# Kernel optimization log

Hardware: AMD Instinct MI355X
Metric: run time of the kernel (lower is better)

## Reference

```python
import jax, jax.numpy as jnp
import numpy as np

B, T, DIN = 256, 2048, 3
H = 128
DOUT = 26


def _slstm_layer(x_seq, W, R, b):
    """sLSTM layer with exponential gating + log-domain stabilizer.
    x_seq: (B, T, Din); W: (4H, Din); R: (4H, H); b: (4H,). Returns (B, T, H)."""
    # input-driven gate preactivations for all timesteps at once
    gx = jnp.einsum('btd,gd->btg', x_seq, W) + b  # (B, T, 4H)
    gx = jnp.swapaxes(gx, 0, 1)                    # (T, B, 4H)
    Bsz = x_seq.shape[0]
    Hd = R.shape[1]
    z0 = jnp.zeros((Bsz, Hd), x_seq.dtype)

    def step(carry, gx_t):
        h, c, n, m = carry
        g = gx_t + h @ R.T                         # (B, 4H)
        it, ft, zt, ot = jnp.split(g, 4, axis=-1)
        m_new = jnp.maximum(ft + m, it)            # stabilizer state
        i = jnp.exp(it - m_new)                    # stabilized exp input gate
        f = jnp.exp(ft + m - m_new)                # stabilized exp forget gate
        z = jnp.tanh(zt)
        o = jax.nn.sigmoid(ot)
        c_new = f * c + i * z
        n_new = f * n + i                          # normalizer state
        h_new = o * (c_new / n_new)
        return (h_new, c_new, n_new, m_new), h_new

    (_, _, _, _), hs = jax.lax.scan(step, (z0, z0, z0, z0), gx)
    return jnp.swapaxes(hs, 0, 1)                  # (B, T, H)


def setup_inputs() -> dict:
    key = jax.random.key(0)
    ks = jax.random.split(key, 12)
    s = 0.1
    x = jax.random.normal(ks[0], (B, T, DIN), dtype=jnp.float32)
    W0 = jax.random.normal(ks[1], (4 * H, DIN), dtype=jnp.float32) * s
    R0 = jax.random.normal(ks[2], (4 * H, H), dtype=jnp.float32) * s
    b0 = jax.random.normal(ks[3], (4 * H,), dtype=jnp.float32) * s
    W1 = jax.random.normal(ks[4], (4 * H, H), dtype=jnp.float32) * s
    R1 = jax.random.normal(ks[5], (4 * H, H), dtype=jnp.float32) * s
    b1 = jax.random.normal(ks[6], (4 * H,), dtype=jnp.float32) * s
    Wmu = jax.random.normal(ks[7], (DOUT, H), dtype=jnp.float32) * s
    bmu = jax.random.normal(ks[8], (DOUT,), dtype=jnp.float32) * s
    Wsig = jax.random.normal(ks[9], (DOUT, H), dtype=jnp.float32) * s
    bsig = jax.random.normal(ks[10], (DOUT,), dtype=jnp.float32) * s
    return {"x": x, "W0": W0, "R0": R0, "b0": b0, "W1": W1, "R1": R1,
            "b1": b1, "Wmu": Wmu, "bmu": bmu, "Wsig": Wsig, "bsig": bsig}


def reference(x, W0, R0, b0, W1, R1, b1, Wmu, bmu, Wsig, bsig):
    h1 = _slstm_layer(x, W0, R0, b0)     # (B, T, H)
    h2 = _slstm_layer(h1, W1, R1, b1)    # (B, T, H)
    last = h2[:, -1, :]                  # (B, H); dropout is identity in eval
    mu = last @ Wmu.T + bmu
    sigma = jax.nn.softplus(last @ Wsig.T + bsig) + 1e-6
    return mu, sigma
```

## Files before the change

### kernel.cpp

```cpp
#include <hip/hip_runtime.h>
#include <cmath>

#define TT    2048
#define HH    128
#define G4    512
#define NDIN  3
#define NDOUT 26
#define NTHR  512

typedef _Float16 h2t __attribute__((ext_vector_type(2)));
typedef _Float16 h8t __attribute__((ext_vector_type(8)));

__device__ __forceinline__ float fdot2(h2t a, h2t b, float c) {
    return __builtin_amdgcn_fdot2(a, b, c, false);
}

union H8u { h8t v; h2t h[4]; };

__device__ __forceinline__ float fast_rcp(float x) { return __builtin_amdgcn_rcpf(x); }

__global__
__attribute__((amdgpu_flat_work_group_size(NTHR, NTHR), amdgpu_waves_per_eu(2, 2)))
void slstm2_kernel(
    const float* __restrict__ x,
    const float* __restrict__ W0, const float* __restrict__ R0, const float* __restrict__ b0,
    const float* __restrict__ W1, const float* __restrict__ R1, const float* __restrict__ b1,
    const float* __restrict__ Wmu, const float* __restrict__ bmu,
    const float* __restrict__ Wsig, const float* __restrict__ bsig,
    float* __restrict__ out, int B)
{
    const int b = blockIdx.x;
    const int j = threadIdx.x;

    __shared__ float xs[TT * NDIN];
    __shared__ __align__(16) _Float16 h1h[HH];
    __shared__ __align__(16) _Float16 h2h[HH];
    __shared__ float g1[G4];
    __shared__ float g2[G4];
    __shared__ float h2f[HH];

    const float* xb = x + (size_t)b * (TT * NDIN);
    #pragma unroll
    for (int r = 0; r < (TT * NDIN) / NTHR; ++r)
        xs[r * NTHR + j] = xb[r * NTHR + j];

    h2t wr0[64], ww1[64], wr1[64];
    {
        const float4* r0p = (const float4*)(R0 + (size_t)j * HH);
        const float4* w1p = (const float4*)(W1 + (size_t)j * HH);
        const float4* r1p = (const float4*)(R1 + (size_t)j * HH);
        #pragma unroll
        for (int k = 0; k < 32; ++k) {
            float4 a = r0p[k];
            h2t t0 = {(_Float16)a.x, (_Float16)a.y};
            h2t t1 = {(_Float16)a.z, (_Float16)a.w};
            wr0[2*k] = t0; wr0[2*k+1] = t1;
            float4 c = w1p[k];
            h2t t2 = {(_Float16)c.x, (_Float16)c.y};
            h2t t3 = {(_Float16)c.z, (_Float16)c.w};
            ww1[2*k] = t2; ww1[2*k+1] = t3;
            float4 d = r1p[k];
            h2t t4 = {(_Float16)d.x, (_Float16)d.y};
            h2t t5 = {(_Float16)d.z, (_Float16)d.w};
            wr1[2*k] = t4; wr1[2*k+1] = t5;
        }
    }
    const float w0a = W0[j*NDIN+0], w0b = W0[j*NDIN+1], w0c = W0[j*NDIN+2];
    const float b0j = b0[j], b1j = b1[j];

    if (j < HH) { h1h[j] = (_Float16)0.f; h2h[j] = (_Float16)0.f; }
    float c_s = 0.f, n_s = 0.f, m_s = 0.f, hlast = 0.f;

    __syncthreads();

    const h8t* h1p = (const h8t*)h1h;
    const h8t* h2p = (const h8t*)h2h;

    for (int t = 0; t <= TT; ++t) {
        const int tc = (t < TT) ? t : (TT - 1);
        const float xv0 = xs[tc*3+0], xv1 = xs[tc*3+1], xv2 = xs[tc*3+2];

        float a0=0.f,a1=0.f,a2=0.f,a3=0.f;
        float d0=0.f,d1=0.f,d2=0.f,d3=0.f;
        float e0=0.f,e1=0.f,e2=0.f,e3=0.f;
        #pragma unroll
        for (int kk = 0; kk < 16; ++kk) {
            H8u u1, u2;
            u1.v = h1p[kk];
            u2.v = h2p[kk];
            a0 = fdot2(wr0[4*kk+0], u1.h[0], a0);
            a1 = fdot2(wr0[4*kk+1], u1.h[1], a1);
            a2 = fdot2(wr0[4*kk+2], u1.h[2], a2);
            a3 = fdot2(wr0[4*kk+3], u1.h[3], a3);
            d0 = fdot2(ww1[4*kk+0], u1.h[0], d0);
            d1 = fdot2(ww1[4*kk+1], u1.h[1], d1);
            d2 = fdot2(ww1[4*kk+2], u1.h[2], d2);
            d3 = fdot2(ww1[4*kk+3], u1.h[3], d3);
            e0 = fdot2(wr1[4*kk+0], u2.h[0], e0);
            e1 = fdot2(wr1[4*kk+1], u2.h[1], e1);
            e2 = fdot2(wr1[4*kk+2], u2.h[2], e2);
            e3 = fdot2(wr1[4*kk+3], u2.h[3], e3);
        }
        g1[j] = b0j + w0a*xv0 + w0b*xv1 + w0c*xv2 + ((a0+a1)+(a2+a3));
        g2[j] = b1j + ((d0+d1)+(d2+d3)) + ((e0+e1)+(e2+e3));
        __syncthreads();

        if (t < TT && j < HH) {
            const float it = g1[j], ft = g1[HH+j], zt = g1[2*HH+j], ot = g1[3*HH+j];
            const float mn = fmaxf(ft + m_s, it);
            const float iv = __expf(it - mn);
            const float fv = __expf(ft + m_s - mn);
            const float tq = __expf(-2.f * fabsf(zt));
            float zv = (1.f - tq) * fast_rcp(1.f + tq);
            zv = (zt < 0.f) ? -zv : zv;
            const float ov = fast_rcp(1.f + __expf(-ot));
            c_s = fv * c_s + iv * zv;
            n_s = fv * n_s + iv;
            m_s = mn;
            const float hv = ov * (c_s * fast_rcp(n_s));
            h1h[j] = (_Float16)hv;
        } else if (t > 0 && j >= HH && j < 2*HH) {
            const int e = j - HH;
            const float it = g2[e], ft = g2[HH+e], zt = g2[2*HH+e], ot = g2[3*HH+e];
            const float mn = fmaxf(ft + m_s, it);
            const float iv = __expf(it - mn);
            const float fv = __expf(ft + m_s - mn);
            const float tq = __expf(-2.f * fabsf(zt));
            float zv = (1.f - tq) * fast_rcp(1.f + tq);
            zv = (zt < 0.f) ? -zv : zv;
            const float ov = fast_rcp(1.f + __expf(-ot));
            c_s = fv * c_s + iv * zv;
            n_s = fv * n_s + iv;
            m_s = mn;
            const float hv = ov * (c_s * fast_rcp(n_s));
            hlast = hv;
            h2h[e] = (_Float16)hv;
        }
        __syncthreads();
    }

    if (j >= HH && j < 2*HH) h2f[j - HH] = hlast;
    __syncthreads();

    if (j < 2 * NDOUT) {
        const int d = (j < NDOUT) ? j : (j - NDOUT);
        const float* Wr = ((j < NDOUT) ? Wmu : Wsig) + (size_t)d * HH;
        float acc = (j < NDOUT) ? bmu[d] : bsig[d];
        #pragma unroll 8
        for (int k = 0; k < HH; ++k) acc += h2f[k] * Wr[k];
        if (j < NDOUT) {
            out[(size_t)b * NDOUT + d] = acc;
        } else {
            const float sp = fmaxf(acc, 0.f) + log1pf(__expf(-fabsf(acc)));
            out[(size_t)B * NDOUT + (size_t)b * NDOUT + d] = sp + 1e-6f;
        }
    }
}

extern "C" void kernel_launch(void* const* d_in, const int* in_sizes, int n_in,
                              void* d_out, int out_size, void* d_ws, size_t ws_size,
                              hipStream_t stream) {
    const float* x    = (const float*)d_in[0];
    const float* W0   = (const float*)d_in[1];
    const float* R0   = (const float*)d_in[2];
    const float* b0   = (const float*)d_in[3];
    const float* W1   = (const float*)d_in[4];
    const float* R1   = (const float*)d_in[5];
    const float* b1   = (const float*)d_in[6];
    const float* Wmu  = (const float*)d_in[7];
    const float* bmu  = (const float*)d_in[8];
    const float* Wsig = (const float*)d_in[9];
    const float* bsig = (const float*)d_in[10];
    float* out = (float*)d_out;

    const int B = in_sizes[0] / (TT * NDIN);

    slstm2_kernel<<<B, NTHR, 0, stream>>>(x, W0, R0, b0, W1, R1, b1,
                                          Wmu, bmu, Wsig, bsig, out, B);
}
```

Measured before the change: 2.430 ms.

## Replace per-thread fdot2 recurrent matvecs with MFMA 16x16x32 f16 tiles

Moves the per-step recurrent matvecs (R0·h1, W1·h1, R1·h2) from per-thread fdot2 loops onto MFMA 16x16x32 instructions, with weight fragments held in registers. Gates are regrouped so the four gates of each hidden unit land together in shared memory. Since the B operand is a single broadcast h vector, most of each MFMA's output columns are redundant and only lane m==0 stores results. The input projection and biases are precomputed into shared tables and applied in the gate stage. The concatenated h buffer serves both layers.

```diff
diff --git a/kernel.cpp b/kernel.cpp
--- a/kernel.cpp
+++ b/kernel.cpp
@@ -3,25 +3,27 @@
 
 #define TT    2048
 #define HH    128
-#define G4    512
 #define NDIN  3
 #define NDOUT 26
 #define NTHR  512
 
-typedef _Float16 h2t __attribute__((ext_vector_type(2)));
-typedef _Float16 h8t __attribute__((ext_vector_type(8)));
-
-__device__ __forceinline__ float fdot2(h2t a, h2t b, float c) {
-    return __builtin_amdgcn_fdot2(a, b, c, false);
+typedef _Float16 f16x8 __attribute__((ext_vector_type(8)));
+typedef float    f32x4 __attribute__((ext_vector_type(4)));
+
+__device__ __forceinline__ float fast_rcp(float x){ return __builtin_amdgcn_rcpf(x); }
+
+__device__ __forceinline__ f16x8 cvt8(const float* __restrict__ p){
+    float4 a = *(const float4*)p;
+    float4 b = *(const float4*)(p+4);
+    f16x8 r;
+    r[0]=(_Float16)a.x; r[1]=(_Float16)a.y; r[2]=(_Float16)a.z; r[3]=(_Float16)a.w;
+    r[4]=(_Float16)b.x; r[5]=(_Float16)b.y; r[6]=(_Float16)b.z; r[7]=(_Float16)b.w;
+    return r;
 }
-
-union H8u { h8t v; h2t h[4]; };
-
-__device__ __forceinline__ float fast_rcp(float x) { return __builtin_amdgcn_rcpf(x); }
 
 __global__
 __attribute__((amdgpu_flat_work_group_size(NTHR, NTHR), amdgpu_waves_per_eu(2, 2)))
-void slstm2_kernel(
+void slstm2_mfma(
     const float* __restrict__ x,
     const float* __restrict__ W0, const float* __restrict__ R0, const float* __restrict__ b0,
     const float* __restrict__ W1, const float* __restrict__ R1, const float* __restrict__ b1,
@@ -29,84 +31,121 @@
     const float* __restrict__ Wsig, const float* __restrict__ bsig,
     float* __restrict__ out, int B)
 {
-    const int b = blockIdx.x;
-    const int j = threadIdx.x;
+    const int b    = blockIdx.x;
+    const int tid  = threadIdx.x;
+    const int wave = tid >> 6;
+    const int lane = tid & 63;
+    const int m    = lane & 15;
+    const int g    = lane >> 4;
 
     __shared__ float xs[TT * NDIN];
-    __shared__ __align__(16) _Float16 h1h[HH];
-    __shared__ __align__(16) _Float16 h2h[HH];
-    __shared__ float g1[G4];
-    __shared__ float g2[G4];
+    __shared__ __align__(16) _Float16 hcat[2 * HH];
+    __shared__ __align__(16) float g1q[HH * 4];
+    __shared__ __align__(16) float g2q[HH * 4];
+    __shared__ __align__(16) float w0g[4][HH * 4];
+    __shared__ __align__(16) float b1qs[HH * 4];
     __shared__ float h2f[HH];
 
     const float* xb = x + (size_t)b * (TT * NDIN);
     #pragma unroll
     for (int r = 0; r < (TT * NDIN) / NTHR; ++r)
-        xs[r * NTHR + j] = xb[r * NTHR + j];
-
-    h2t wr0[64], ww1[64], wr1[64];
-    {
-        const float4* r0p = (const float4*)(R0 + (size_t)j * HH);
-        const float4* w1p = (const float4*)(W1 + (size_t)j * HH);
-        const float4* r1p = (const float4*)(R1 + (size_t)j * HH);
-        #pragma unroll
-        for (int k = 0; k < 32; ++k) {
-            float4 a = r0p[k];
-            h2t t0 = {(_Float16)a.x, (_Float16)a.y};
-            h2t t1 = {(_Float16)a.z, (_Float16)a.w};
-            wr0[2*k] = t0; wr0[2*k+1] = t1;
-            float4 c = w1p[k];
-            h2t t2 = {(_Float16)c.x, (_Float16)c.y};
-            h2t t3 = {(_Float16)c.z, (_Float16)c.w};
-            ww1[2*k] = t2; ww1[2*k+1] = t3;
-            float4 d = r1p[k];
-            h2t t4 = {(_Float16)d.x, (_Float16)d.y};
-            h2t t5 = {(_Float16)d.z, (_Float16)d.w};
-            wr1[2*k] = t4; wr1[2*k+1] = t5;
-        }
-    }
-    const float w0a = W0[j*NDIN+0], w0b = W0[j*NDIN+1], w0c = W0[j*NDIN+2];
-    const float b0j = b0[j], b1j = b1[j];
-
-    if (j < HH) { h1h[j] = (_Float16)0.f; h2h[j] = (_Float16)0.f; }
+        xs[r * NTHR + tid] = xb[r * NTHR + tid];
+
+    if (tid < HH) {
+        #pragma unroll
+        for (int q = 0; q < 4; ++q) {
+            w0g[q][tid*4+0] = W0[(q*HH + tid)*NDIN + 0];
+            w0g[q][tid*4+1] = W0[(q*HH + tid)*NDIN + 1];
+            w0g[q][tid*4+2] = W0[(q*HH + tid)*NDIN + 2];
+            w0g[q][tid*4+3] = b0[q*HH + tid];
+            b1qs[tid*4+q]   = b1[q*HH + tid];
+        }
+        hcat[tid] = (_Float16)0.f;
+        hcat[HH + tid] = (_Float16)0.f;
+    }
+
+    f16x8 a1[4][4];
+    f16x8 a2[4][8];
+    #pragma unroll
+    for (int tl = 0; tl < 4; ++tl) {
+        const int e = (wave*4 + tl)*4 + (m >> 2);
+        const int q = m & 3;
+        const size_t row = (size_t)(q*HH + e);
+        #pragma unroll
+        for (int kt = 0; kt < 4; ++kt)
+            a1[tl][kt] = cvt8(R0 + row*HH + kt*32 + g*8);
+        #pragma unroll
+        for (int kt = 0; kt < 4; ++kt)
+            a2[tl][kt] = cvt8(W1 + row*HH + kt*32 + g*8);
+        #pragma unroll
+        for (int kt = 0; kt < 4; ++kt)
+            a2[tl][4+kt] = cvt8(R1 + row*HH + kt*32 + g*8);
+    }
+
     float c_s = 0.f, n_s = 0.f, m_s = 0.f, hlast = 0.f;
-
     __syncthreads();
 
-    const h8t* h1p = (const h8t*)h1h;
-    const h8t* h2p = (const h8t*)h2h;
-
     for (int t = 0; t <= TT; ++t) {
-        const int tc = (t < TT) ? t : (TT - 1);
-        const float xv0 = xs[tc*3+0], xv1 = xs[tc*3+1], xv2 = xs[tc*3+2];
-
-        float a0=0.f,a1=0.f,a2=0.f,a3=0.f;
-        float d0=0.f,d1=0.f,d2=0.f,d3=0.f;
-        float e0=0.f,e1=0.f,e2=0.f,e3=0.f;
-        #pragma unroll
-        for (int kk = 0; kk < 16; ++kk) {
-            H8u u1, u2;
-            u1.v = h1p[kk];
-            u2.v = h2p[kk];
-            a0 = fdot2(wr0[4*kk+0], u1.h[0], a0);
-            a1 = fdot2(wr0[4*kk+1], u1.h[1], a1);
-            a2 = fdot2(wr0[4*kk+2], u1.h[2], a2);
-            a3 = fdot2(wr0[4*kk+3], u1.h[3], a3);
-            d0 = fdot2(ww1[4*kk+0], u1.h[0], d0);
-            d1 = fdot2(ww1[4*kk+1], u1.h[1], d1);
-            d2 = fdot2(ww1[4*kk+2], u1.h[2], d2);
-            d3 = fdot2(ww1[4*kk+3], u1.h[3], d3);
-            e0 = fdot2(wr1[4*kk+0], u2.h[0], e0);
-            e1 = fdot2(wr1[4*kk+1], u2.h[1], e1);
-            e2 = fdot2(wr1[4*kk+2], u2.h[2], e2);
-            e3 = fdot2(wr1[4*kk+3], u2.h[3], e3);
-        }
-        g1[j] = b0j + w0a*xv0 + w0b*xv1 + w0c*xv2 + ((a0+a1)+(a2+a3));
-        g2[j] = b1j + ((d0+d1)+(d2+d3)) + ((e0+e1)+(e2+e3));
+        f16x8 bf[4];
+        #pragma unroll
+        for (int kt = 0; kt < 4; ++kt)
+            bf[kt] = *(const f16x8*)(hcat + kt*32 + g*8);
+
+        f32x4 cL1[4];
+        #pragma unroll
+        for (int tl = 0; tl < 4; ++tl) cL1[tl] = f32x4{0.f,0.f,0.f,0.f};
+        #pragma unroll
+        for (int kt = 0; kt < 4; ++kt) {
+            #pragma unroll
+            for (int tl = 0; tl < 4; ++tl)
+                cL1[tl] = __builtin_amdgcn_mfma_f32_16x16x32_f16(a1[tl][kt], bf[kt], cL1[tl], 0, 0, 0);
+        }
+        if (m == 0) {
+            #pragma unroll
+            for (int tl = 0; tl < 4; ++tl) {
+                const int e = (wave*4 + tl)*4 + g;
+                *(f32x4*)(g1q + e*4) = cL1[tl];
+            }
+        }
+
+        f32x4 cL2[4];
+        #pragma unroll
+        for (int tl = 0; tl < 4; ++tl) cL2[tl] = f32x4{0.f,0.f,0.f,0.f};
+        #pragma unroll
+        for (int kt = 0; kt < 4; ++kt) {
+            #pragma unroll
+            for (int tl = 0; tl < 4; ++tl)
+                cL2[tl] = __builtin_amdgcn_mfma_f32_16x16x32_f16(a2[tl][kt], bf[kt], cL2[tl], 0, 0, 0);
+        }
+        #pragma unroll
+        for (int kt = 0; kt < 4; ++kt)
+            bf[kt] = *(const f16x8*)(hcat + HH + kt*32 + g*8);
+        #pragma unroll
+        for (int kt = 0; kt < 4; ++kt) {
+            #pragma unroll
+            for (int tl = 0; tl < 4; ++tl)
+                cL2[tl] = __builtin_amdgcn_mfma_f32_16x16x32_f16(a2[tl][4+kt], bf[kt], cL2[tl], 0, 0, 0);
+        }
+        if (m == 0) {
+            #pragma unroll
+            for (int tl = 0; tl < 4; ++tl) {
+                const int e = (wave*4 + tl)*4 + g;
+                *(f32x4*)(g2q + e*4) = cL2[tl];
+            }
+        }
         __syncthreads();
 
-        if (t < TT && j < HH) {
-            const float it = g1[j], ft = g1[HH+j], zt = g1[2*HH+j], ot = g1[3*HH+j];
+        if (t < TT && tid < HH) {
+            f32x4 qd = *(const f32x4*)(g1q + tid*4);
+            const float x0 = xs[t*3+0], x1 = xs[t*3+1], x2 = xs[t*3+2];
+            f32x4 wi = *(const f32x4*)(&w0g[0][tid*4]);
+            f32x4 wf = *(const f32x4*)(&w0g[1][tid*4]);
+            f32x4 wz = *(const f32x4*)(&w0g[2][tid*4]);
+            f32x4 wo = *(const f32x4*)(&w0g[3][tid*4]);
+            const float it = qd[0] + wi[0]*x0 + wi[1]*x1 + wi[2]*x2 + wi[3];
+            const float ft = qd[1] + wf[0]*x0 + wf[1]*x1 + wf[2]*x2 + wf[3];
+            const float zt = qd[2] + wz[0]*x0 + wz[1]*x1 + wz[2]*x2 + wz[3];
+            const float ot = qd[3] + wo[0]*x0 + wo[1]*x1 + wo[2]*x2 + wo[3];
             const float mn = fmaxf(ft + m_s, it);
             const float iv = __expf(it - mn);
             const float fv = __expf(ft + m_s - mn);
@@ -118,10 +157,15 @@
             n_s = fv * n_s + iv;
             m_s = mn;
             const float hv = ov * (c_s * fast_rcp(n_s));
-            h1h[j] = (_Float16)hv;
-        } else if (t > 0 && j >= HH && j < 2*HH) {
-            const int e = j - HH;
-            const float it = g2[e], ft = g2[HH+e], zt = g2[2*HH+e], ot = g2[3*HH+e];
+            hcat[tid] = (_Float16)hv;
+        } else if (t > 0 && tid >= HH && tid < 2*HH) {
+            const int e = tid - HH;
+            f32x4 qd = *(const f32x4*)(g2q + e*4);
+            f32x4 bb = *(const f32x4*)(b1qs + e*4);
+            const float it = qd[0] + bb[0];
+            const float ft = qd[1] + bb[1];
+            const float zt = qd[2] + bb[2];
+            const float ot = qd[3] + bb[3];
             const float mn = fmaxf(ft + m_s, it);
             const float iv = __expf(it - mn);
             const float fv = __expf(ft + m_s - mn);
@@ -134,21 +178,21 @@
             m_s = mn;
             const float hv = ov * (c_s * fast_rcp(n_s));
             hlast = hv;
-            h2h[e] = (_Float16)hv;
+            hcat[HH + e] = (_Float16)hv;
         }
         __syncthreads();
     }
 
-    if (j >= HH && j < 2*HH) h2f[j - HH] = hlast;
+    if (tid >= HH && tid < 2*HH) h2f[tid - HH] = hlast;
     __syncthreads();
 
-    if (j < 2 * NDOUT) {
-        const int d = (j < NDOUT) ? j : (j - NDOUT);
-        const float* Wr = ((j < NDOUT) ? Wmu : Wsig) + (size_t)d * HH;
-        float acc = (j < NDOUT) ? bmu[d] : bsig[d];
+    if (tid < 2 * NDOUT) {
+        const int d = (tid < NDOUT) ? tid : (tid - NDOUT);
+        const float* Wr = ((tid < NDOUT) ? Wmu : Wsig) + (size_t)d * HH;
+        float acc = (tid < NDOUT) ? bmu[d] : bsig[d];
         #pragma unroll 8
         for (int k = 0; k < HH; ++k) acc += h2f[k] * Wr[k];
-        if (j < NDOUT) {
+        if (tid < NDOUT) {
             out[(size_t)b * NDOUT + d] = acc;
         } else {
             const float sp = fmaxf(acc, 0.f) + log1pf(__expf(-fabsf(acc)));
@@ -175,6 +219,6 @@
 
     const int B = in_sizes[0] / (TT * NDIN);
 
-    slstm2_kernel<<<B, NTHR, 0, stream>>>(x, W0, R0, b0, W1, R1, b1,
-                                          Wmu, bmu, Wsig, bsig, out, B);
+    slstm2_mfma<<<B, NTHR, 0, stream>>>(x, W0, R0, b0, W1, R1, b1,
+                                        Wmu, bmu, Wsig, bsig, out, B);
 }
```

Result: slower. 2.734 ms (+12.5%).
